# Optimization experiments

Hardware: AMD Instinct MI355X
Metric: run time of the kernel (lower is better)

Reference implementation:

```python
import jax, jax.numpy as jnp
import numpy as np

OBJECT_NUM = 512
ATTRIBUTES_NUM = 8
E_DIMS = 256


def setup_inputs() -> dict:
    key = jax.random.key(0)
    k1, k2 = jax.random.split(key)
    x = jax.random.normal(k1, (64, 2048), dtype=jnp.float32)
    E_absolute_position = jax.random.normal(k2, (OBJECT_NUM, E_DIMS), dtype=jnp.float32)
    return {"x": x, "E_absolute_position": E_absolute_position}


def reference(x, E_absolute_position):
    batch_size, seq_len = x.shape[0], x.shape[1]
    # token index -> object index via floor division (same as int(token/attributes_num))
    idx = jnp.arange(seq_len) // ATTRIBUTES_NUM          # [S]
    rows = E_absolute_position[idx]                       # [S, E]
    out = jnp.broadcast_to(rows[None, :, :], (batch_size, seq_len, E_DIMS))
    return out
```

## Files before the change

kernel.cpp:

```cpp
#include <hip/hip_runtime.h>


typedef float floatx4 __attribute__((ext_vector_type(4)));

constexpr unsigned BATCH           = 64;
constexpr unsigned SEQ             = 2048;
constexpr unsigned EDIM            = 256;
constexpr unsigned VEC_PER_ROW     = EDIM / 4;
constexpr unsigned PLANE_VEC       = SEQ * VEC_PER_ROW;
constexpr unsigned BLOCK           = 256;
constexpr unsigned BATCH_PER_BLOCK = 16;

__global__ __launch_bounds__(BLOCK)
void ape_broadcast_kernel(const floatx4* __restrict__ E, floatx4* __restrict__ out) {
    unsigned v   = blockIdx.x * BLOCK + threadIdx.x;
    unsigned e4  = v & (VEC_PER_ROW - 1);
    unsigned s   = v >> 6;
    unsigned obj = s >> 3;

    floatx4 val = E[obj * VEC_PER_ROW + e4];

    unsigned b0 = blockIdx.y * BATCH_PER_BLOCK;
    floatx4* p  = out + (size_t)b0 * PLANE_VEC + v;
#pragma unroll
    for (unsigned i = 0; i < BATCH_PER_BLOCK; ++i) {
        __builtin_nontemporal_store(val, p);
        p += PLANE_VEC;
    }
}

extern "C" void kernel_launch(void* const* d_in, const int* in_sizes, int n_in,
                              void* d_out, int out_size, void* d_ws, size_t ws_size,
                              hipStream_t stream) {
    const floatx4* E = (const floatx4*)d_in[1];
    floatx4* out     = (floatx4*)d_out;

    dim3 grid(PLANE_VEC / BLOCK,
              BATCH / BATCH_PER_BLOCK);
    ape_broadcast_kernel<<<grid, dim3(BLOCK), 0, stream>>>(E, out);
}
```

Baseline: 140.5 us.

## Assign contiguous output spans per wave with fewer persistent-style blocks

Replaces the 2D grid where each thread wrote the same vector across 16 batch planes with a 1D grid of 512 blocks, where each wave writes a contiguous 64 KiB span covering 8 objects. Each E row is loaded once per 8 output rows. The nontemporal stores are replaced by regular stores. This aims for sequential write streams per wave, at the risk of lower occupancy and more L2 pressure from cached stores.

```diff
diff --git a/kernel.cpp b/kernel.cpp
--- a/kernel.cpp
+++ b/kernel.cpp
@@ -3,29 +3,37 @@
 
 typedef float floatx4 __attribute__((ext_vector_type(4)));
 
-constexpr unsigned BATCH           = 64;
-constexpr unsigned SEQ             = 2048;
-constexpr unsigned EDIM            = 256;
-constexpr unsigned VEC_PER_ROW     = EDIM / 4;
-constexpr unsigned PLANE_VEC       = SEQ * VEC_PER_ROW;
-constexpr unsigned BLOCK           = 256;
-constexpr unsigned BATCH_PER_BLOCK = 16;
+constexpr unsigned BATCH        = 64;
+constexpr unsigned SEQ          = 2048;
+constexpr unsigned EDIM         = 256;
+constexpr unsigned VEC_PER_ROW  = EDIM / 4;
+constexpr unsigned TOTAL_VEC    = BATCH * SEQ * VEC_PER_ROW;
+constexpr unsigned BLOCK        = 256;
+constexpr unsigned GRID         = 512;
+constexpr unsigned WAVE_VEC     = TOTAL_VEC / (GRID * 4);
+constexpr unsigned ROWS_PER_WAVE = WAVE_VEC / VEC_PER_ROW;
+constexpr unsigned OBJS_PER_WAVE = ROWS_PER_WAVE / 8;
+
+static_assert(WAVE_VEC * GRID * 4 == TOTAL_VEC, "exact cover");
+static_assert((SEQ * VEC_PER_ROW) % WAVE_VEC == 0, "no plane crossing");
 
 __global__ __launch_bounds__(BLOCK)
 void ape_broadcast_kernel(const floatx4* __restrict__ E, floatx4* __restrict__ out) {
-    unsigned v   = blockIdx.x * BLOCK + threadIdx.x;
-    unsigned e4  = v & (VEC_PER_ROW - 1);
-    unsigned s   = v >> 6;
-    unsigned obj = s >> 3;
+    unsigned lane = threadIdx.x & 63;
+    unsigned wave = blockIdx.x * (BLOCK / 64) + (threadIdx.x >> 6);
+    unsigned base = wave * WAVE_VEC;
+    unsigned s0   = (base >> 6) & (SEQ - 1);
+    unsigned obj0 = s0 >> 3;
 
-    floatx4 val = E[obj * VEC_PER_ROW + e4];
-
-    unsigned b0 = blockIdx.y * BATCH_PER_BLOCK;
-    floatx4* p  = out + (size_t)b0 * PLANE_VEC + v;
+    floatx4* p = out + base + lane;
 #pragma unroll
-    for (unsigned i = 0; i < BATCH_PER_BLOCK; ++i) {
-        __builtin_nontemporal_store(val, p);
-        p += PLANE_VEC;
+    for (unsigned oj = 0; oj < OBJS_PER_WAVE; ++oj) {
+        floatx4 val = E[(obj0 + oj) * VEC_PER_ROW + lane];
+#pragma unroll
+        for (unsigned r = 0; r < 8; ++r) {
+            *p = val;
+            p += VEC_PER_ROW;
+        }
     }
 }
 
@@ -34,8 +42,5 @@
                               hipStream_t stream) {
     const floatx4* E = (const floatx4*)d_in[1];
     floatx4* out     = (floatx4*)d_out;
-
-    dim3 grid(PLANE_VEC / BLOCK,
-              BATCH / BATCH_PER_BLOCK);
-    ape_broadcast_kernel<<<grid, dim3(BLOCK), 0, stream>>>(E, out);
+    ape_broadcast_kernel<<<GRID, BLOCK, 0, stream>>>(E, out);
 }
```

Result: faster. 133.5 us (-5.0%).
